# Kernel optimization log

Hardware: AMD Instinct MI355X
Metric: run time of the kernel (lower is better)

The kernel has to match this reference:

```python
import jax, jax.numpy as jnp
import numpy as np

B, S, D, H = 4, 2048, 1024, 16
DK = D // H
WINDOW = 256
GLOBAL = 16
NEG_INF = float(np.finfo(np.float32).min)


def local_window_mask(seq_len, window, global_tokens):
    # 0 where attention allowed, -inf where |i-j| > window and neither i nor j is a global token
    i = jnp.arange(seq_len)[:, None]
    j = jnp.arange(seq_len)[None, :]
    is_global = (i < global_tokens) | (j < global_tokens)
    out_of_window = jnp.abs(i - j) > window
    return jnp.where(out_of_window & ~is_global, NEG_INF, 0.0).astype(jnp.float32)


def setup_inputs() -> dict:
    key = jax.random.key(0)
    ks = jax.random.split(key, 8)
    std = 1.0 / np.sqrt(D)
    return {
        "q": jax.random.normal(ks[0], (B, S, D), jnp.float32),
        "k": jax.random.normal(ks[1], (B, S, D), jnp.float32),
        "v": jax.random.normal(ks[2], (B, S, D), jnp.float32),
        "attn_mask": jnp.zeros((B, S), jnp.float32),
        "wq": jax.random.normal(ks[3], (D, D), jnp.float32) * std,
        "bq": jnp.zeros((D,), jnp.float32),
        "wk": jax.random.normal(ks[4], (D, D), jnp.float32) * std,
        "bk": jnp.zeros((D,), jnp.float32),
        "wv": jax.random.normal(ks[5], (D, D), jnp.float32) * std,
        "bv": jnp.zeros((D,), jnp.float32),
        "wo": jax.random.normal(ks[6], (D, D), jnp.float32) * std,
        "bo": jnp.zeros((D,), jnp.float32),
    }


def reference(q, k, v, attn_mask, wq, bq, wk, bk, wv, bv, wo, bo):
    b, s, d = q.shape
    # projections (x @ W + b)
    Q = (q @ wq + bq).reshape(b, s, H, DK).transpose(0, 2, 1, 3)  # b h s dk
    K = (k @ wk + bk).reshape(b, s, H, DK).transpose(0, 2, 1, 3)
    V = (v @ wv + bv).reshape(b, s, H, DK).transpose(0, 2, 1, 3)

    scale = 1.0 / np.sqrt(DK)
    scores = jnp.einsum("bhqd,bhkd->bhqk", Q, K) * scale  # b h s s
    # additive key mask broadcast over query positions: attn_mask[:, None, None, :]
    scores = scores + attn_mask[:, None, None, :]
    scores = scores + local_window_mask(s, WINDOW, GLOBAL)[None, None, :, :]
    probs = jax.nn.softmax(scores, axis=-1)
    out = jnp.einsum("bhqk,bhkd->bhqd", probs, V)  # b h s dk
    out = out.transpose(0, 2, 1, 3).reshape(b, s, d)
    return out @ wo + bo
```

## Files before the change

kernel.cpp:

```cpp
#include <hip/hip_runtime.h>


#define B_   4
#define S_   2048
#define D_   1024
#define H_   16
#define DK_  64
#define WIN_ 256
#define GLB_ 16

typedef __attribute__((ext_vector_type(8))) short bf16x8;
typedef __attribute__((ext_vector_type(4))) float floatx4;

__device__ __forceinline__ unsigned short f2bf(float x) {
  unsigned u = __float_as_uint(x);
  unsigned r = u + 0x7FFFu + ((u >> 16) & 1u);
  return (unsigned short)(r >> 16);
}
__device__ __forceinline__ float bf2f(unsigned short h) {
  return __uint_as_float(((unsigned)h) << 16);
}
__device__ __forceinline__ void gload_lds16(const void* g, void* l) {
  __builtin_amdgcn_global_load_lds(
      (const __attribute__((address_space(1))) unsigned int*)g,
      (__attribute__((address_space(3))) unsigned int*)l, 16, 0, 0);
}

__global__ void split_bf16(const float* __restrict__ x,
                           unsigned short* __restrict__ hi,
                           unsigned short* __restrict__ lo)
{
  const int i = blockIdx.x * 256 + threadIdx.x;
  const float4 v = ((const float4*)x)[i];
  unsigned short h0 = f2bf(v.x), h1 = f2bf(v.y), h2 = f2bf(v.z), h3 = f2bf(v.w);
  unsigned short l0 = f2bf(v.x - bf2f(h0)), l1 = f2bf(v.y - bf2f(h1));
  unsigned short l2 = f2bf(v.z - bf2f(h2)), l3 = f2bf(v.w - bf2f(h3));
  unsigned long long hp = (unsigned long long)h0 | ((unsigned long long)h1 << 16)
                        | ((unsigned long long)h2 << 32) | ((unsigned long long)h3 << 48);
  unsigned long long lp = (unsigned long long)l0 | ((unsigned long long)l1 << 16)
                        | ((unsigned long long)l2 << 32) | ((unsigned long long)l3 << 48);
  ((unsigned long long*)hi)[i] = hp;
  ((unsigned long long*)lo)[i] = lp;
}

__global__ void wtsplit(const float* __restrict__ W,
                        unsigned short* __restrict__ hiT,
                        unsigned short* __restrict__ loT)
{
  __shared__ float t[32][33];
  const int bx = blockIdx.x * 32;
  const int by = blockIdx.y * 32;
  const int c = threadIdx.x & 31;
  const int r0 = (threadIdx.x >> 5) * 4;
#pragma unroll
  for (int i = 0; i < 4; ++i)
    t[r0 + i][c] = W[(size_t)(by + r0 + i) * 1024 + bx + c];
  __syncthreads();
#pragma unroll
  for (int i = 0; i < 4; ++i) {
    const int r = r0 + i;
    const float val = t[c][r];
    const unsigned short h = f2bf(val);
    hiT[(size_t)(bx + r) * 1024 + by + c] = h;
    loT[(size_t)(bx + r) * 1024 + by + c] = f2bf(val - bf2f(h));
  }
}

__global__ __launch_bounds__(256, 2) void gemm_mfma(
    const unsigned short* __restrict__ Ahi, const unsigned short* __restrict__ Alo,
    const unsigned short* __restrict__ WThi, const unsigned short* __restrict__ WTlo,
    const float* __restrict__ bias, float* __restrict__ Cf,
    unsigned short* __restrict__ Chi, unsigned short* __restrict__ Clo, int mode)
{
  __shared__ unsigned short AsH[4096], AsL[4096], WsH[4096], WsL[4096];
  const int tid = threadIdx.x;
  const int w = tid >> 6, lane = tid & 63;
  const int wr = w >> 1, wc = w & 1;
  const int bm = blockIdx.y * 128, bn = blockIdx.x * 128;
  const int lrow = lane & 15, lk8 = (lane >> 4) * 8;

  floatx4 acc[4][4];
#pragma unroll
  for (int t = 0; t < 4; ++t)
#pragma unroll
    for (int u = 0; u < 4; ++u) acc[t][u] = (floatx4){0.f, 0.f, 0.f, 0.f};

  const unsigned short* gsrc;
  unsigned short* lbase;
  int growbase;
  if      (w == 0) { gsrc = Ahi;  lbase = AsH; growbase = bm; }
  else if (w == 1) { gsrc = Alo;  lbase = AsL; growbase = bm; }
  else if (w == 2) { gsrc = WThi; lbase = WsH; growbase = bn; }
  else             { gsrc = WTlo; lbase = WsL; growbase = bn; }

  for (int k0 = 0; k0 < 1024; k0 += 32) {
    __syncthreads();
#pragma unroll
    for (int g = 0; g < 8; ++g) {
      const unsigned short* gp =
          gsrc + (size_t)(growbase + g * 16 + lrow) * 1024 + k0 + lk8;
      gload_lds16(gp, lbase + g * 512);
    }
    __syncthreads();

    bf16x8 ah[4], al[4], bh[4], bl[4];
#pragma unroll
    for (int t = 0; t < 4; ++t) {
      ah[t] = *(const bf16x8*)&AsH[(wr * 4 + t) * 512 + lane * 8];
      al[t] = *(const bf16x8*)&AsL[(wr * 4 + t) * 512 + lane * 8];
    }
#pragma unroll
    for (int u = 0; u < 4; ++u) {
      bh[u] = *(const bf16x8*)&WsH[(wc * 4 + u) * 512 + lane * 8];
      bl[u] = *(const bf16x8*)&WsL[(wc * 4 + u) * 512 + lane * 8];
    }
#pragma unroll
    for (int t = 0; t < 4; ++t)
#pragma unroll
      for (int u = 0; u < 4; ++u) {
        acc[t][u] = __builtin_amdgcn_mfma_f32_16x16x32_bf16(al[t], bh[u], acc[t][u], 0, 0, 0);
        acc[t][u] = __builtin_amdgcn_mfma_f32_16x16x32_bf16(ah[t], bl[u], acc[t][u], 0, 0, 0);
        acc[t][u] = __builtin_amdgcn_mfma_f32_16x16x32_bf16(ah[t], bh[u], acc[t][u], 0, 0, 0);
      }
  }

  float bs[4];
#pragma unroll
  for (int u = 0; u < 4; ++u) bs[u] = bias[bn + wc * 64 + u * 16 + lrow];

#pragma unroll
  for (int t = 0; t < 4; ++t)
#pragma unroll
    for (int r = 0; r < 4; ++r) {
      const int row = bm + wr * 64 + t * 16 + (lane >> 4) * 4 + r;
#pragma unroll
      for (int u = 0; u < 4; ++u) {
        const int col = bn + wc * 64 + u * 16 + lrow;
        const float val = acc[t][u][r] + bs[u];
        if (mode == 0) {
          Cf[(size_t)row * 1024 + col] = val;
        } else {
          const int bb = row >> 11, s = row & 2047;
          const int hh = col >> 6, dk = col & 63;
          if (mode == 1) {
            const size_t a = ((size_t)(bb * H_ + hh) * S_ + s) * DK_ + dk;
            const unsigned short hv = f2bf(val);
            Chi[a] = hv;
            Clo[a] = f2bf(val - bf2f(hv));
          } else {
            Chi[((size_t)(bb * H_ + hh) * DK_ + dk) * S_ + s] = f2bf(val);
          }
        }
      }
    }
}

__global__ __launch_bounds__(256, 4) void attn_mfma(
    const unsigned short* __restrict__ Qhi, const unsigned short* __restrict__ Qlo,
    const unsigned short* __restrict__ Khi, const unsigned short* __restrict__ Klo,
    const unsigned short* __restrict__ Vt,  const float* __restrict__ amask,
    unsigned short* __restrict__ AOhi, unsigned short* __restrict__ AOlo)
{
  __shared__ unsigned short lds[16384];

  const int tid = threadIdx.x;
  const int w = tid >> 6, lane = tid & 63;
  const int quad = lane >> 4, lm = lane & 15;
  const int qt = blockIdx.x, h = blockIdx.y, b = blockIdx.z;
  const int i0 = qt * 64;

  const size_t hb = (size_t)(b * H_ + h) * S_ * DK_;
  const unsigned short* Qhih = Qhi + hb;
  const unsigned short* Qloh = Qlo + hb;
  const unsigned short* Khih = Khi + hb;
  const unsigned short* Kloh = Klo + hb;
  const unsigned short* Vth  = Vt  + hb;

  const int myrow = i0 + w * 16 + lm;

  bf16x8 bqh[2], bql[2];
#pragma unroll
  for (int p = 0; p < 2; ++p) {
    const size_t qa = (size_t)myrow * DK_ + p * 32 + quad * 8;
    bqh[p] = *(const bf16x8*)(Qhih + qa);
    bql[p] = *(const bf16x8*)(Qloh + qa);
  }

  floatx4 acc[4];
  float m_i = -1e30f, l_i = 0.f;
#pragma unroll
  for (int u = 0; u < 4; ++u) acc[u] = (floatx4){0.f, 0.f, 0.f, 0.f};

  int start, t_lo, t_hi;
  if (qt == 0) { start = 0; t_lo = 0; t_hi = 31; }
  else {
    start = -1;
    t_lo = qt - 4 < 1 ? 1 : qt - 4;
    t_hi = qt + 4 > 31 ? 31 : qt + 4;
  }

  unsigned short* Pw = &lds[12288 + w * 1024];
  const bool iglb = (myrow < GLB_);

  for (int tt = start; tt <= t_hi; ++tt) {
    if (tt >= 0 && tt < t_lo) continue;
    const int kt = (tt < 0) ? 0 : tt;
    const int k0 = kt * 64;

    __syncthreads();
    for (int e = w; e < 24; e += 4) {
      const int op = e >> 3, cc = e & 7, g = cc >> 1, hf = cc & 1;
      unsigned short* ldst = &lds[op * 4096 + g * 1024 + hf * 512];
      const unsigned short* gp;
      if (op == 0)      gp = Khih + (size_t)(k0 + g * 16 + lm) * DK_ + (hf * 4 + quad) * 8;
      else if (op == 1) gp = Kloh + (size_t)(k0 + g * 16 + lm) * DK_ + (hf * 4 + quad) * 8;
      else              gp = Vth + (size_t)(g * 16 + lm) * S_ + k0 + (hf * 4 + quad) * 8;
      gload_lds16(gp, ldst);
    }
    __syncthreads();

    floatx4 sc[4];
#pragma unroll
    for (int u = 0; u < 4; ++u) sc[u] = (floatx4){0.f, 0.f, 0.f, 0.f};
#pragma unroll
    for (int u = 0; u < 4; ++u)
#pragma unroll
      for (int p = 0; p < 2; ++p) {
        const bf16x8 kh = *(const bf16x8*)&lds[       u * 1024 + p * 512 + lane * 8];
        const bf16x8 kl = *(const bf16x8*)&lds[4096 + u * 1024 + p * 512 + lane * 8];
        sc[u] = __builtin_amdgcn_mfma_f32_16x16x32_bf16(kh, bql[p], sc[u], 0, 0, 0);
        sc[u] = __builtin_amdgcn_mfma_f32_16x16x32_bf16(kl, bqh[p], sc[u], 0, 0, 0);
        sc[u] = __builtin_amdgcn_mfma_f32_16x16x32_bf16(kh, bqh[p], sc[u], 0, 0, 0);
      }

    float mx = -1e30f;
#pragma unroll
    for (int u = 0; u < 4; ++u) {
      const float4 amv = *(const float4*)(amask + b * S_ + k0 + u * 16 + quad * 4);
      const float amr[4] = {amv.x, amv.y, amv.z, amv.w};
#pragma unroll
      for (int r = 0; r < 4; ++r) {
        const int j = k0 + u * 16 + quad * 4 + r;
        const int diff = myrow - j;
        const bool ok = (diff <= WIN_ && diff >= -WIN_) || iglb || (j < GLB_);
        const float sv = ok ? fmaf(sc[u][r], 0.125f, amr[r]) : -1e30f;
        sc[u][r] = sv;
        mx = fmaxf(mx, sv);
      }
    }
    mx = fmaxf(mx, __shfl_xor(mx, 16));
    mx = fmaxf(mx, __shfl_xor(mx, 32));

    const float mn = fmaxf(m_i, mx);
    const float alpha = __expf(m_i - mn);
    m_i = mn;
    float rsum = 0.f;
#pragma unroll
    for (int u = 0; u < 4; ++u)
#pragma unroll
      for (int r = 0; r < 4; ++r) {
        const float pv = __expf(sc[u][r] - mn);
        sc[u][r] = pv;
        rsum += pv;
      }
    rsum += __shfl_xor(rsum, 16);
    rsum += __shfl_xor(rsum, 32);
    l_i = l_i * alpha + rsum;
#pragma unroll
    for (int u = 0; u < 4; ++u) {
      acc[u][0] *= alpha; acc[u][1] *= alpha;
      acc[u][2] *= alpha; acc[u][3] *= alpha;
    }

#pragma unroll
    for (int u = 0; u < 4; ++u) {
      const unsigned long long pk =
          (unsigned long long)f2bf(sc[u][0])
        | ((unsigned long long)f2bf(sc[u][1]) << 16)
        | ((unsigned long long)f2bf(sc[u][2]) << 32)
        | ((unsigned long long)f2bf(sc[u][3]) << 48);
      *(unsigned long long*)&Pw[(u * 2 + (quad >> 1)) * 128 + lm * 8 + (quad & 1) * 4] = pk;
    }

#pragma unroll
    for (int p = 0; p < 2; ++p) {
      const bf16x8 pf = *(const bf16x8*)&Pw[p * 512 + lane * 8];
#pragma unroll
      for (int u = 0; u < 4; ++u) {
        const bf16x8 vf = *(const bf16x8*)&lds[8192 + u * 1024 + p * 512 + lane * 8];
        acc[u] = __builtin_amdgcn_mfma_f32_16x16x32_bf16(vf, pf, acc[u], 0, 0, 0);
      }
    }
  }

  const float linv = 1.0f / l_i;
  const size_t rowa = (size_t)(b * S_ + myrow) * D_ + h * DK_;
#pragma unroll
  for (int u = 0; u < 4; ++u) {
    float vv[4];
    unsigned short hv[4];
#pragma unroll
    for (int r = 0; r < 4; ++r) { vv[r] = acc[u][r] * linv; hv[r] = f2bf(vv[r]); }
    unsigned long long hp = (unsigned long long)hv[0] | ((unsigned long long)hv[1] << 16)
                          | ((unsigned long long)hv[2] << 32) | ((unsigned long long)hv[3] << 48);
    unsigned long long lp = 0;
#pragma unroll
    for (int r = 0; r < 4; ++r)
      lp |= ((unsigned long long)f2bf(vv[r] - bf2f(hv[r]))) << (16 * r);
    *(unsigned long long*)&AOhi[rowa + u * 16 + quad * 4] = hp;
    *(unsigned long long*)&AOlo[rowa + u * 16 + quad * 4] = lp;
  }
}

#define BM 128
#define BN 128
#define BK 16

__global__ __launch_bounds__(256, 2) void gemm_f32(
    const float* __restrict__ A, const float* __restrict__ W,
    const float* __restrict__ bias, float* __restrict__ C, int mode)
{
  __shared__ float As[BK][BM + 4];
  __shared__ float Bs[BK][BN + 4];
  const int tid = threadIdx.x;
  const int bm = blockIdx.y * BM;
  const int bn = blockIdx.x * BN;
  const int tx = tid & 15;
  const int ty = tid >> 4;
  const int K = 1024, N = 1024;

  float acc[8][8];
#pragma unroll
  for (int i = 0; i < 8; ++i)
#pragma unroll
    for (int j = 0; j < 8; ++j) acc[i][j] = 0.f;

  const int arow = tid >> 2;
  const int acol = (tid & 3) * 4;
  const int brow = tid >> 5;
  const int bcol = (tid & 31) * 4;

  for (int k0 = 0; k0 < K; k0 += BK) {
    float4 a0 = *(const float4*)(A + (size_t)(bm + arow) * K + k0 + acol);
    float4 a1 = *(const float4*)(A + (size_t)(bm + arow + 64) * K + k0 + acol);
    float4 b0 = *(const float4*)(W + (size_t)(k0 + brow) * N + bn + bcol);
    float4 b1 = *(const float4*)(W + (size_t)(k0 + brow + 8) * N + bn + bcol);
    __syncthreads();
    As[acol + 0][arow] = a0.x; As[acol + 1][arow] = a0.y;
    As[acol + 2][arow] = a0.z; As[acol + 3][arow] = a0.w;
    As[acol + 0][arow + 64] = a1.x; As[acol + 1][arow + 64] = a1.y;
    As[acol + 2][arow + 64] = a1.z; As[acol + 3][arow + 64] = a1.w;
    *(float4*)&Bs[brow][bcol]     = b0;
    *(float4*)&Bs[brow + 8][bcol] = b1;
    __syncthreads();
#pragma unroll
    for (int kk = 0; kk < BK; ++kk) {
      float a[8], bb[8];
      float4 t;
      t = *(float4*)&As[kk][ty * 8];     a[0]=t.x; a[1]=t.y; a[2]=t.z; a[3]=t.w;
      t = *(float4*)&As[kk][ty * 8 + 4]; a[4]=t.x; a[5]=t.y; a[6]=t.z; a[7]=t.w;
      t = *(float4*)&Bs[kk][tx * 8];     bb[0]=t.x; bb[1]=t.y; bb[2]=t.z; bb[3]=t.w;
      t = *(float4*)&Bs[kk][tx * 8 + 4]; bb[4]=t.x; bb[5]=t.y; bb[6]=t.z; bb[7]=t.w;
#pragma unroll
      for (int i = 0; i < 8; ++i)
#pragma unroll
        for (int j = 0; j < 8; ++j)
          acc[i][j] = fmaf(a[i], bb[j], acc[i][j]);
    }
  }

  const float4 bias0 = *(const float4*)(bias + bn + tx * 8);
  const float4 bias1 = *(const float4*)(bias + bn + tx * 8 + 4);
  if (mode == 0) {
#pragma unroll
    for (int i = 0; i < 8; ++i) {
      const int m = bm + ty * 8 + i;
      float* dst = C + (size_t)m * 1024 + bn + tx * 8;
      *(float4*)dst = make_float4(acc[i][0] + bias0.x, acc[i][1] + bias0.y,
                                  acc[i][2] + bias0.z, acc[i][3] + bias0.w);
      *(float4*)(dst + 4) = make_float4(acc[i][4] + bias1.x, acc[i][5] + bias1.y,
                                        acc[i][6] + bias1.z, acc[i][7] + bias1.w);
    }
  } else {
    const int ncol = bn + tx * 8;
    const int h  = ncol >> 6;
    const int dk = ncol & 63;
#pragma unroll
    for (int i = 0; i < 8; ++i) {
      const int m = bm + ty * 8 + i;
      const int bb2 = m >> 11;
      const int s  = m & 2047;
      float* dst = C + ((size_t)(bb2 * H_ + h) * S_ + s) * DK_ + dk;
      *(float4*)dst = make_float4(acc[i][0] + bias0.x, acc[i][1] + bias0.y,
                                  acc[i][2] + bias0.z, acc[i][3] + bias0.w);
      *(float4*)(dst + 4) = make_float4(acc[i][4] + bias1.x, acc[i][5] + bias1.y,
                                        acc[i][6] + bias1.z, acc[i][7] + bias1.w);
    }
  }
}

__global__ __launch_bounds__(256, 2) void attn_v3(
    const float* __restrict__ Qp, const float* __restrict__ Kp,
    const float* __restrict__ Vp, const float* __restrict__ amask,
    float* __restrict__ AO)
{
  __shared__ float Qs[64][68], Ks[64][68], Vs[64][68], Ps[64][68];

  const int tid = threadIdx.x;
  const int qt = blockIdx.x;
  const int h  = blockIdx.y;
  const int b  = blockIdx.z;
  const int i0 = qt * 64;
  const int tr = tid >> 4;
  const int tc = tid & 15;

  const size_t head_off = (size_t)(b * H_ + h) * S_ * DK_;
  const float* Qh = Qp + head_off;
  const float* Kh = Kp + head_off;
  const float* Vh = Vp + head_off;

#pragma unroll
  for (int r = 0; r < 4; ++r) {
    const int f = tid + r * 256;
    const int row = f >> 4, col = (f & 15) * 4;
    *(float4*)&Qs[row][col] = *(const float4*)(Qh + (size_t)(i0 + row) * DK_ + col);
  }

  float m_i[4], l_i[4];
  float4 acc[4];
#pragma unroll
  for (int i = 0; i < 4; ++i) {
    m_i[i] = -1e30f; l_i[i] = 0.f;
    acc[i] = make_float4(0.f, 0.f, 0.f, 0.f);
  }

  int start, t_lo, t_hi;
  if (qt == 0) { start = 0; t_lo = 0; t_hi = 31; }
  else {
    start = -1;
    t_lo = qt - 4 < 1 ? 1 : qt - 4;
    t_hi = qt + 4 > 31 ? 31 : qt + 4;
  }

  for (int tt = start; tt <= t_hi; ++tt) {
    if (tt >= 0 && tt < t_lo) continue;
    const int kt = (tt < 0) ? 0 : tt;
    const int k0 = kt * 64;

    __syncthreads();
#pragma unroll
    for (int r = 0; r < 4; ++r) {
      const int f = tid + r * 256;
      const int row = f >> 4, col = (f & 15) * 4;
      *(float4*)&Ks[row][col] = *(const float4*)(Kh + (size_t)(k0 + row) * DK_ + col);
      *(float4*)&Vs[row][col] = *(const float4*)(Vh + (size_t)(k0 + row) * DK_ + col);
    }
    __syncthreads();

    float am[4];
#pragma unroll
    for (int u = 0; u < 4; ++u) am[u] = amask[b * S_ + k0 + tc + 16 * u];

    float s[4][4];
#pragma unroll
    for (int i = 0; i < 4; ++i)
#pragma unroll
      for (int u = 0; u < 4; ++u) s[i][u] = 0.f;
#pragma unroll
    for (int d4 = 0; d4 < 16; ++d4) {
      const float4 k0v = *(float4*)&Ks[tc     ][d4 * 4];
      const float4 k1v = *(float4*)&Ks[tc + 16][d4 * 4];
      const float4 k2v = *(float4*)&Ks[tc + 32][d4 * 4];
      const float4 k3v = *(float4*)&Ks[tc + 48][d4 * 4];
#pragma unroll
      for (int i = 0; i < 4; ++i) {
        const float4 q = *(float4*)&Qs[tr * 4 + i][d4 * 4];
        s[i][0] += q.x*k0v.x + q.y*k0v.y + q.z*k0v.z + q.w*k0v.w;
        s[i][1] += q.x*k1v.x + q.y*k1v.y + q.z*k1v.z + q.w*k1v.w;
        s[i][2] += q.x*k2v.x + q.y*k2v.y + q.z*k2v.z + q.w*k2v.w;
        s[i][3] += q.x*k3v.x + q.y*k3v.y + q.z*k3v.z + q.w*k3v.w;
      }
    }

#pragma unroll
    for (int i = 0; i < 4; ++i) {
      const int irow = i0 + tr * 4 + i;
#pragma unroll
      for (int u = 0; u < 4; ++u) {
        const int j = k0 + tc + 16 * u;
        const int diff = irow - j;
        const bool allowed = (diff <= WIN_ && diff >= -WIN_) || (irow < GLB_) || (j < GLB_);
        s[i][u] = allowed ? fmaf(s[i][u], 0.125f, am[u]) : -1e30f;
      }
    }

    float mt[4];
#pragma unroll
    for (int i = 0; i < 4; ++i)
      mt[i] = fmaxf(fmaxf(s[i][0], s[i][1]), fmaxf(s[i][2], s[i][3]));
#pragma unroll
    for (int st = 1; st <= 8; st <<= 1)
#pragma unroll
      for (int i = 0; i < 4; ++i)
        mt[i] = fmaxf(mt[i], __shfl_xor(mt[i], st));

    float alpha[4], rs[4];
#pragma unroll
    for (int i = 0; i < 4; ++i) {
      const float mn = fmaxf(m_i[i], mt[i]);
      alpha[i] = __expf(m_i[i] - mn);
      m_i[i] = mn;
      float r = 0.f;
#pragma unroll
      for (int u = 0; u < 4; ++u) {
        s[i][u] = __expf(s[i][u] - mn);
        r += s[i][u];
      }
      rs[i] = r;
    }
#pragma unroll
    for (int st = 1; st <= 8; st <<= 1)
#pragma unroll
      for (int i = 0; i < 4; ++i)
        rs[i] += __shfl_xor(rs[i], st);
#pragma unroll
    for (int i = 0; i < 4; ++i) {
      l_i[i] = l_i[i] * alpha[i] + rs[i];
      acc[i].x *= alpha[i]; acc[i].y *= alpha[i];
      acc[i].z *= alpha[i]; acc[i].w *= alpha[i];
    }

#pragma unroll
    for (int u = 0; u < 4; ++u)
      *(float4*)&Ps[tc + 16 * u][tr * 4] =
          make_float4(s[0][u], s[1][u], s[2][u], s[3][u]);
    __syncthreads();

#pragma unroll 4
    for (int j = 0; j < 64; ++j) {
      const float4 p4 = *(float4*)&Ps[j][tr * 4];
      const float4 v4 = *(float4*)&Vs[j][tc * 4];
      acc[0].x = fmaf(p4.x, v4.x, acc[0].x); acc[0].y = fmaf(p4.x, v4.y, acc[0].y);
      acc[0].z = fmaf(p4.x, v4.z, acc[0].z); acc[0].w = fmaf(p4.x, v4.w, acc[0].w);
      acc[1].x = fmaf(p4.y, v4.x, acc[1].x); acc[1].y = fmaf(p4.y, v4.y, acc[1].y);
      acc[1].z = fmaf(p4.y, v4.z, acc[1].z); acc[1].w = fmaf(p4.y, v4.w, acc[1].w);
      acc[2].x = fmaf(p4.z, v4.x, acc[2].x); acc[2].y = fmaf(p4.z, v4.y, acc[2].y);
      acc[2].z = fmaf(p4.z, v4.z, acc[2].z); acc[2].w = fmaf(p4.z, v4.w, acc[2].w);
      acc[3].x = fmaf(p4.w, v4.x, acc[3].x); acc[3].y = fmaf(p4.w, v4.y, acc[3].y);
      acc[3].z = fmaf(p4.w, v4.z, acc[3].z); acc[3].w = fmaf(p4.w, v4.w, acc[3].w);
    }
  }

#pragma unroll
  for (int i = 0; i < 4; ++i) {
    const float linv = 1.0f / l_i[i];
    const int row = i0 + tr * 4 + i;
    float* dst = AO + ((size_t)b * S_ + row) * D_ + h * DK_ + tc * 4;
    *(float4*)dst = make_float4(acc[i].x * linv, acc[i].y * linv,
                                acc[i].z * linv, acc[i].w * linv);
  }
}

extern "C" void kernel_launch(void* const* d_in, const int* in_sizes, int n_in,
                              void* d_out, int out_size, void* d_ws, size_t ws_size,
                              hipStream_t stream) {
  const float* q  = (const float*)d_in[0];
  const float* k  = (const float*)d_in[1];
  const float* v  = (const float*)d_in[2];
  const float* am = (const float*)d_in[3];
  const float* wq = (const float*)d_in[4];
  const float* bq = (const float*)d_in[5];
  const float* wk = (const float*)d_in[6];
  const float* bk = (const float*)d_in[7];
  const float* wv = (const float*)d_in[8];
  const float* bv = (const float*)d_in[9];
  const float* wo = (const float*)d_in[10];
  const float* bo = (const float*)d_in[11];
  float* out = (float*)d_out;

  const size_t PER = (size_t)B_ * H_ * S_ * DK_;
  const size_t NEED = 138412032;

  if (ws_size >= NEED) {
    unsigned short* us = (unsigned short*)d_ws;
    unsigned short* ACTh = us;
    unsigned short* ACTl = us + PER;
    unsigned short* Qhi  = us + 2 * PER;
    unsigned short* Qlo  = us + 3 * PER;
    unsigned short* Khi  = us + 4 * PER;
    unsigned short* Klo  = us + 5 * PER;
    unsigned short* Vtp  = us + 6 * PER;
    unsigned short* WHI  = us + 7 * PER;
    unsigned short* WLO  = WHI + 1048576;

    const int sgrid = (int)(PER / 4 / 256);
    dim3 wgrid(32, 32);
    dim3 ggrid(8, 64);

    split_bf16<<<sgrid, 256, 0, stream>>>(q, ACTh, ACTl);
    wtsplit<<<wgrid, 256, 0, stream>>>(wq, WHI, WLO);
    gemm_mfma<<<ggrid, 256, 0, stream>>>(ACTh, ACTl, WHI, WLO, bq, nullptr, Qhi, Qlo, 1);

    split_bf16<<<sgrid, 256, 0, stream>>>(k, ACTh, ACTl);
    wtsplit<<<wgrid, 256, 0, stream>>>(wk, WHI, WLO);
    gemm_mfma<<<ggrid, 256, 0, stream>>>(ACTh, ACTl, WHI, WLO, bk, nullptr, Khi, Klo, 1);

    split_bf16<<<sgrid, 256, 0, stream>>>(v, ACTh, ACTl);
    wtsplit<<<wgrid, 256, 0, stream>>>(wv, WHI, WLO);
    gemm_mfma<<<ggrid, 256, 0, stream>>>(ACTh, ACTl, WHI, WLO, bv, nullptr, Vtp, nullptr, 2);

    attn_mfma<<<dim3(S_ / 64, H_, B_), 256, 0, stream>>>(
        Qhi, Qlo, Khi, Klo, Vtp, am, ACTh, ACTl);

    wtsplit<<<wgrid, 256, 0, stream>>>(wo, WHI, WLO);
    gemm_mfma<<<ggrid, 256, 0, stream>>>(ACTh, ACTl, WHI, WLO, bo, out, nullptr, nullptr, 0);
  } else {
    float* Qp = (float*)d_ws;
    float* Kp = Qp + PER;
    float* Vp = Kp + PER;
    float* AOf = Vp + PER;
    dim3 gg(D_ / BN, (B_ * S_) / BM);
    gemm_f32<<<gg, 256, 0, stream>>>(q, wq, bq, Qp, 1);
    gemm_f32<<<gg, 256, 0, stream>>>(k, wk, bk, Kp, 1);
    gemm_f32<<<gg, 256, 0, stream>>>(v, wv, bv, Vp, 1);
    attn_v3<<<dim3(S_ / 64, H_, B_), 256, 0, stream>>>(Qp, Kp, Vp, am, AOf);
    gemm_f32<<<gg, 256, 0, stream>>>(AOf, wo, bo, out, 0);
  }
}
```

Measured before the change: 752.3 us.

## Double-buffer K tiles in LDS and load V fragments directly into registers

The attention loop now keeps two LDS buffers for the K hi/lo tiles. It prefetches the next key tile while the current one is consumed, which removes the second barrier per iteration. V fragments are read straight from global memory into registers instead of being staged through LDS. The qt==0 / skip-iteration logic becomes a compact tile count, and launch bounds drop to 3 blocks per CU to fit the larger LDS footprint. Risks: lower occupancy, and in-order vmcnt waits on the V loads may also stall on the prefetch, limiting overlap.

Measured after the change: 941.3 us. +25.1%, slower.

```diff
diff --git a/kernel.cpp b/kernel.cpp
--- a/kernel.cpp
+++ b/kernel.cpp
@@ -155,13 +155,28 @@
     }
 }
 
-__global__ __launch_bounds__(256, 4) void attn_mfma(
+__device__ __forceinline__ void stage_k(
+    const unsigned short* __restrict__ Khih, const unsigned short* __restrict__ Kloh,
+    unsigned short* __restrict__ dst, int k0, int w, int lm, int quad)
+{
+#pragma unroll
+  for (int ii = 0; ii < 4; ++ii) {
+    const int e = w + ii * 4;
+    const int op = e >> 3;
+    const int c = e & 7, g = c >> 1, hf = c & 1;
+    const unsigned short* gp =
+        (op ? Kloh : Khih) + (size_t)(k0 + g * 16 + lm) * DK_ + (hf * 4 + quad) * 8;
+    gload_lds16(gp, dst + op * 4096 + c * 512);
+  }
+}
+
+__global__ __launch_bounds__(256, 3) void attn_mfma(
     const unsigned short* __restrict__ Qhi, const unsigned short* __restrict__ Qlo,
     const unsigned short* __restrict__ Khi, const unsigned short* __restrict__ Klo,
     const unsigned short* __restrict__ Vt,  const float* __restrict__ amask,
     unsigned short* __restrict__ AOhi, unsigned short* __restrict__ AOlo)
 {
-  __shared__ unsigned short lds[16384];
+  __shared__ unsigned short lds[20480];
 
   const int tid = threadIdx.x;
   const int w = tid >> 6, lane = tid & 63;
@@ -191,34 +206,38 @@
 #pragma unroll
   for (int u = 0; u < 4; ++u) acc[u] = (floatx4){0.f, 0.f, 0.f, 0.f};
 
-  int start, t_lo, t_hi;
-  if (qt == 0) { start = 0; t_lo = 0; t_hi = 31; }
-  else {
-    start = -1;
-    t_lo = qt - 4 < 1 ? 1 : qt - 4;
-    t_hi = qt + 4 > 31 ? 31 : qt + 4;
-  }
-
-  unsigned short* Pw = &lds[12288 + w * 1024];
+  int t_lo = qt - 4 < 1 ? 1 : qt - 4;
+  int t_hi = qt + 4 > 31 ? 31 : qt + 4;
+  const int nt = (qt == 0) ? 32 : (t_hi - t_lo + 2);
+
+  unsigned short* Pw = &lds[16384 + w * 1024];
   const bool iglb = (myrow < GLB_);
 
-  for (int tt = start; tt <= t_hi; ++tt) {
-    if (tt >= 0 && tt < t_lo) continue;
-    const int kt = (tt < 0) ? 0 : tt;
+  {
+    const int kt0 = 0;
+    stage_k(Khih, Kloh, lds, kt0 * 64, w, lm, quad);
+  }
+  int cur = 0;
+
+  for (int i = 0; i < nt; ++i) {
+    const int kt = (qt == 0) ? i : ((i == 0) ? 0 : (t_lo + i - 1));
     const int k0 = kt * 64;
 
     __syncthreads();
-    for (int e = w; e < 24; e += 4) {
-      const int op = e >> 3, cc = e & 7, g = cc >> 1, hf = cc & 1;
-      unsigned short* ldst = &lds[op * 4096 + g * 1024 + hf * 512];
-      const unsigned short* gp;
-      if (op == 0)      gp = Khih + (size_t)(k0 + g * 16 + lm) * DK_ + (hf * 4 + quad) * 8;
-      else if (op == 1) gp = Kloh + (size_t)(k0 + g * 16 + lm) * DK_ + (hf * 4 + quad) * 8;
-      else              gp = Vth + (size_t)(g * 16 + lm) * S_ + k0 + (hf * 4 + quad) * 8;
-      gload_lds16(gp, ldst);
-    }
-    __syncthreads();
-
+
+    if (i + 1 < nt) {
+      const int ktn = (qt == 0) ? (i + 1) : (t_lo + i);
+      stage_k(Khih, Kloh, lds + (1 - cur) * 8192, ktn * 64, w, lm, quad);
+    }
+
+    bf16x8 vf[4][2];
+#pragma unroll
+    for (int u = 0; u < 4; ++u)
+#pragma unroll
+      for (int p = 0; p < 2; ++p)
+        vf[u][p] = *(const bf16x8*)(Vth + (size_t)(u * 16 + lm) * S_ + k0 + (p * 4 + quad) * 8);
+
+    const unsigned short* Kc = lds + cur * 8192;
     floatx4 sc[4];
 #pragma unroll
     for (int u = 0; u < 4; ++u) sc[u] = (floatx4){0.f, 0.f, 0.f, 0.f};
@@ -226,8 +245,8 @@
     for (int u = 0; u < 4; ++u)
 #pragma unroll
       for (int p = 0; p < 2; ++p) {
-        const bf16x8 kh = *(const bf16x8*)&lds[       u * 1024 + p * 512 + lane * 8];
-        const bf16x8 kl = *(const bf16x8*)&lds[4096 + u * 1024 + p * 512 + lane * 8];
+        const bf16x8 kh = *(const bf16x8*)&Kc[       u * 1024 + p * 512 + lane * 8];
+        const bf16x8 kl = *(const bf16x8*)&Kc[4096 + u * 1024 + p * 512 + lane * 8];
         sc[u] = __builtin_amdgcn_mfma_f32_16x16x32_bf16(kh, bql[p], sc[u], 0, 0, 0);
         sc[u] = __builtin_amdgcn_mfma_f32_16x16x32_bf16(kl, bqh[p], sc[u], 0, 0, 0);
         sc[u] = __builtin_amdgcn_mfma_f32_16x16x32_bf16(kh, bqh[p], sc[u], 0, 0, 0);
@@ -286,11 +305,11 @@
     for (int p = 0; p < 2; ++p) {
       const bf16x8 pf = *(const bf16x8*)&Pw[p * 512 + lane * 8];
 #pragma unroll
-      for (int u = 0; u < 4; ++u) {
-        const bf16x8 vf = *(const bf16x8*)&lds[8192 + u * 1024 + p * 512 + lane * 8];
-        acc[u] = __builtin_amdgcn_mfma_f32_16x16x32_bf16(vf, pf, acc[u], 0, 0, 0);
-      }
-    }
+      for (int u = 0; u < 4; ++u)
+        acc[u] = __builtin_amdgcn_mfma_f32_16x16x32_bf16(vf[u][p], pf, acc[u], 0, 0, 0);
+    }
+
+    cur ^= 1;
   }
 
   const float linv = 1.0f / l_i;
```

## Make each wave own a 16-row strip loading K/V directly to registers

Applied to the files above, without the earlier changes.

The attention kernel stops staging K and V tiles through shared memory with block-wide barriers. Each wave now handles its own 16-query strip with its own tight key-tile range and loads K hi/lo and V fragments straight from global memory into registers. A fast path skips the per-element window mask on tiles known to lie fully inside the window. This removes the barriers and the wasted key tiles per strip, but drops K/V reuse across the four waves of a block, and the larger register arrays force lower occupancy (launch bounds 4 to 2).

After: 751.3 us. About the same (-0.1%).

```diff
diff --git a/kernel.cpp b/kernel.cpp
--- a/kernel.cpp
+++ b/kernel.cpp
@@ -155,19 +155,20 @@
     }
 }
 
-__global__ __launch_bounds__(256, 4) void attn_mfma(
+__global__ __launch_bounds__(256, 2) void attn_mfma(
     const unsigned short* __restrict__ Qhi, const unsigned short* __restrict__ Qlo,
     const unsigned short* __restrict__ Khi, const unsigned short* __restrict__ Klo,
     const unsigned short* __restrict__ Vt,  const float* __restrict__ amask,
     unsigned short* __restrict__ AOhi, unsigned short* __restrict__ AOlo)
 {
-  __shared__ unsigned short lds[16384];
+  __shared__ unsigned short Pall[4][1024];
 
   const int tid = threadIdx.x;
   const int w = tid >> 6, lane = tid & 63;
   const int quad = lane >> 4, lm = lane & 15;
-  const int qt = blockIdx.x, h = blockIdx.y, b = blockIdx.z;
-  const int i0 = qt * 64;
+  const int strip = blockIdx.x * 4 + w;
+  const int h = blockIdx.y, b = blockIdx.z;
+  const int i0w = strip * 16;
 
   const size_t hb = (size_t)(b * H_ + h) * S_ * DK_;
   const unsigned short* Qhih = Qhi + hb;
@@ -176,7 +177,7 @@
   const unsigned short* Kloh = Klo + hb;
   const unsigned short* Vth  = Vt  + hb;
 
-  const int myrow = i0 + w * 16 + lm;
+  const int myrow = i0w + lm;
 
   bf16x8 bqh[2], bql[2];
 #pragma unroll
@@ -191,33 +192,31 @@
 #pragma unroll
   for (int u = 0; u < 4; ++u) acc[u] = (floatx4){0.f, 0.f, 0.f, 0.f};
 
-  int start, t_lo, t_hi;
-  if (qt == 0) { start = 0; t_lo = 0; t_hi = 31; }
-  else {
-    start = -1;
-    t_lo = qt - 4 < 1 ? 1 : qt - 4;
-    t_hi = qt + 4 > 31 ? 31 : qt + 4;
-  }
-
-  unsigned short* Pw = &lds[12288 + w * 1024];
-  const bool iglb = (myrow < GLB_);
-
-  for (int tt = start; tt <= t_hi; ++tt) {
-    if (tt >= 0 && tt < t_lo) continue;
-    const int kt = (tt < 0) ? 0 : tt;
+  int t_lo = (i0w - WIN_) >> 6; if (t_lo < 1) t_lo = 1;
+  int t_hi = (i0w + 15 + WIN_) >> 6; if (t_hi > 31) t_hi = 31;
+  const int nt = (i0w == 0) ? 32 : (t_hi - t_lo + 2);
+
+  unsigned short* Pw = Pall[w];
+
+  for (int it = 0; it < nt; ++it) {
+    const int kt = (i0w == 0) ? it : ((it == 0) ? 0 : (t_lo + it - 1));
     const int k0 = kt * 64;
 
-    __syncthreads();
-    for (int e = w; e < 24; e += 4) {
-      const int op = e >> 3, cc = e & 7, g = cc >> 1, hf = cc & 1;
-      unsigned short* ldst = &lds[op * 4096 + g * 1024 + hf * 512];
-      const unsigned short* gp;
-      if (op == 0)      gp = Khih + (size_t)(k0 + g * 16 + lm) * DK_ + (hf * 4 + quad) * 8;
-      else if (op == 1) gp = Kloh + (size_t)(k0 + g * 16 + lm) * DK_ + (hf * 4 + quad) * 8;
-      else              gp = Vth + (size_t)(g * 16 + lm) * S_ + k0 + (hf * 4 + quad) * 8;
-      gload_lds16(gp, ldst);
-    }
-    __syncthreads();
+    bf16x8 kh[4][2], kl[4][2];
+#pragma unroll
+    for (int u = 0; u < 4; ++u)
+#pragma unroll
+      for (int p = 0; p < 2; ++p) {
+        const size_t ka = (size_t)(k0 + u * 16 + lm) * DK_ + p * 32 + quad * 8;
+        kh[u][p] = *(const bf16x8*)(Khih + ka);
+        kl[u][p] = *(const bf16x8*)(Kloh + ka);
+      }
+    bf16x8 vt[4][2];
+#pragma unroll
+    for (int u = 0; u < 4; ++u)
+#pragma unroll
+      for (int p = 0; p < 2; ++p)
+        vt[u][p] = *(const bf16x8*)(Vth + (size_t)(u * 16 + lm) * S_ + k0 + p * 32 + quad * 8);
 
     floatx4 sc[4];
 #pragma unroll
@@ -226,26 +225,41 @@
     for (int u = 0; u < 4; ++u)
 #pragma unroll
       for (int p = 0; p < 2; ++p) {
-        const bf16x8 kh = *(const bf16x8*)&lds[       u * 1024 + p * 512 + lane * 8];
-        const bf16x8 kl = *(const bf16x8*)&lds[4096 + u * 1024 + p * 512 + lane * 8];
-        sc[u] = __builtin_amdgcn_mfma_f32_16x16x32_bf16(kh, bql[p], sc[u], 0, 0, 0);
-        sc[u] = __builtin_amdgcn_mfma_f32_16x16x32_bf16(kl, bqh[p], sc[u], 0, 0, 0);
-        sc[u] = __builtin_amdgcn_mfma_f32_16x16x32_bf16(kh, bqh[p], sc[u], 0, 0, 0);
-      }
-
+        sc[u] = __builtin_amdgcn_mfma_f32_16x16x32_bf16(kh[u][p], bql[p], sc[u], 0, 0, 0);
+        sc[u] = __builtin_amdgcn_mfma_f32_16x16x32_bf16(kl[u][p], bqh[p], sc[u], 0, 0, 0);
+        sc[u] = __builtin_amdgcn_mfma_f32_16x16x32_bf16(kh[u][p], bqh[p], sc[u], 0, 0, 0);
+      }
+
+    const bool easy = (i0w == 0) ||
+                      (kt >= 1 && k0 >= i0w - (WIN_ - 15) && k0 <= i0w + (WIN_ - 63));
     float mx = -1e30f;
-#pragma unroll
-    for (int u = 0; u < 4; ++u) {
-      const float4 amv = *(const float4*)(amask + b * S_ + k0 + u * 16 + quad * 4);
-      const float amr[4] = {amv.x, amv.y, amv.z, amv.w};
-#pragma unroll
-      for (int r = 0; r < 4; ++r) {
-        const int j = k0 + u * 16 + quad * 4 + r;
-        const int diff = myrow - j;
-        const bool ok = (diff <= WIN_ && diff >= -WIN_) || iglb || (j < GLB_);
-        const float sv = ok ? fmaf(sc[u][r], 0.125f, amr[r]) : -1e30f;
-        sc[u][r] = sv;
-        mx = fmaxf(mx, sv);
+    if (easy) {
+#pragma unroll
+      for (int u = 0; u < 4; ++u) {
+        const float4 amv = *(const float4*)(amask + b * S_ + k0 + u * 16 + quad * 4);
+        const float amr[4] = {amv.x, amv.y, amv.z, amv.w};
+#pragma unroll
+        for (int r = 0; r < 4; ++r) {
+          const float sv = fmaf(sc[u][r], 0.125f, amr[r]);
+          sc[u][r] = sv;
+          mx = fmaxf(mx, sv);
+        }
+      }
+    } else {
+      const bool iglb = (myrow < GLB_);
+#pragma unroll
+      for (int u = 0; u < 4; ++u) {
+        const float4 amv = *(const float4*)(amask + b * S_ + k0 + u * 16 + quad * 4);
+        const float amr[4] = {amv.x, amv.y, amv.z, amv.w};
+#pragma unroll
+        for (int r = 0; r < 4; ++r) {
+          const int j = k0 + u * 16 + quad * 4 + r;
+          const int diff = myrow - j;
+          const bool ok = (diff <= WIN_ && diff >= -WIN_) || iglb || (j < GLB_);
+          const float sv = ok ? fmaf(sc[u][r], 0.125f, amr[r]) : -1e30f;
+          sc[u][r] = sv;
+          mx = fmaxf(mx, sv);
+        }
       }
     }
     mx = fmaxf(mx, __shfl_xor(mx, 16));
@@ -286,10 +300,8 @@
     for (int p = 0; p < 2; ++p) {
       const bf16x8 pf = *(const bf16x8*)&Pw[p * 512 + lane * 8];
 #pragma unroll
-      for (int u = 0; u < 4; ++u) {
-        const bf16x8 vf = *(const bf16x8*)&lds[8192 + u * 1024 + p * 512 + lane * 8];
-        acc[u] = __builtin_amdgcn_mfma_f32_16x16x32_bf16(vf, pf, acc[u], 0, 0, 0);
-      }
+      for (int u = 0; u < 4; ++u)
+        acc[u] = __builtin_amdgcn_mfma_f32_16x16x32_bf16(vt[u][p], pf, acc[u], 0, 0, 0);
     }
   }
 
@@ -609,7 +621,7 @@
     wtsplit<<<wgrid, 256, 0, stream>>>(wv, WHI, WLO);
     gemm_mfma<<<ggrid, 256, 0, stream>>>(ACTh, ACTl, WHI, WLO, bv, nullptr, Vtp, nullptr, 2);
 
-    attn_mfma<<<dim3(S_ / 64, H_, B_), 256, 0, stream>>>(
+    attn_mfma<<<dim3(32, H_, B_), 256, 0, stream>>>(
         Qhi, Qlo, Khi, Klo, Vtp, am, ACTh, ACTl);
 
     wtsplit<<<wgrid, 256, 0, stream>>>(wo, WHI, WLO);
```
